# Kernel optimization log

Measured on AMD Instinct MI355X. Metric: run time of the kernel, lower is better.

## Reference

```python
import jax, jax.numpy as jnp
import numpy as np
from jax import lax

D_MODEL = 1024
D_FF = 4096
NUM_EXPERTS = 24
TOP_K = 2
B, S = 2, 2048


def setup_inputs() -> dict:
    key = jax.random.key(0)
    ks = jax.random.split(key, 5)
    x = jax.random.normal(ks[0], (B, S, D_MODEL), dtype=jnp.float32)
    gate_w = jax.random.normal(ks[1], (D_MODEL, NUM_EXPERTS), dtype=jnp.float32) * 0.02
    gate_b = jnp.zeros((NUM_EXPERTS,), dtype=jnp.float32)
    w1 = jax.random.normal(ks[2], (NUM_EXPERTS, D_MODEL, D_FF), dtype=jnp.float32) * 0.02
    b1 = jnp.zeros((NUM_EXPERTS, D_FF), dtype=jnp.float32)
    w2 = jax.random.normal(ks[3], (NUM_EXPERTS, D_FF, D_MODEL), dtype=jnp.float32) * 0.02
    b2 = jnp.zeros((NUM_EXPERTS, D_MODEL), dtype=jnp.float32)
    return {"x": x, "gate_w": gate_w, "gate_b": gate_b,
            "w1": w1, "b1": b1, "w2": w2, "b2": b2}


def reference(x, gate_w, gate_b, w1, b1, w2, b2):
    b, s, d = x.shape
    t = b * s
    xf = x.reshape(t, d)  # [T, d]
    scores = xf @ gate_w + gate_b  # [T, E]
    top_val, top_idx = lax.top_k(scores, TOP_K)  # [T, k]
    prob = jax.nn.softmax(top_val, axis=-1)  # softmax over the top-k logits
    # scatter top-k probabilities into dense per-expert combine weights [T, E]
    combine = jnp.zeros((t, NUM_EXPERTS), dtype=x.dtype)
    combine = combine.at[jnp.arange(t)[:, None], top_idx].add(prob)

    def body(acc, expert):
        w1e, b1e, w2e, b2e, ce = expert  # ce: [T]
        h = jax.nn.gelu(xf @ w1e + b1e, approximate=False)  # exact GELU as torch default
        y = h @ w2e + b2e  # [T, d]
        return acc + ce[:, None] * y, None

    out, _ = lax.scan(body, jnp.zeros_like(xf), (w1, b1, w2, b2, combine.T))
    return out.reshape(b, s, d)
```

## Files before the change

kernel.cpp:

```cpp
#include <hip/hip_runtime.h>
#include <math.h>

#define DM 1024
#define DF 4096
#define NE 24
#define T_TOK 4096
#define T2 (T_TOK*2)

#define BM 128
#define BN 64
#define BK 64
#define MTILES 8
#define NK1 (DM / BK)
#define NK2 (DF / BK)

typedef __attribute__((ext_vector_type(4))) float f32x4;
typedef __attribute__((ext_vector_type(8))) short s16x8;

static __device__ __forceinline__ unsigned short f2bf(float f) {
    unsigned int u = __float_as_uint(f);
    unsigned int r = u + 0x7fffu + ((u >> 16) & 1u);
    return (unsigned short)(r >> 16);
}

static __device__ __forceinline__ unsigned int cvtpk(float lo, float hi) {
    unsigned int r;
    asm("v_cvt_pk_bf16_f32 %0, %1, %2" : "=v"(r) : "v"(lo), "v"(hi));
    return r;
}

#define GLL(gsrc, ldst)                                                          \
    __builtin_amdgcn_global_load_lds(                                            \
        (const __attribute__((address_space(1))) void*)(gsrc),                   \
        (__attribute__((address_space(3))) void*)(ldst), 16, 0, 0)


__global__ void k_transpose_gw(const float* __restrict__ gw, float* __restrict__ gwT) {
    int e = blockIdx.x;
    for (int d = threadIdx.x; d < DM; d += blockDim.x)
        gwT[e * DM + d] = gw[d * NE + e];
}

__global__ void k_gate(const float* __restrict__ x, const float* __restrict__ gwT,
                       const float* __restrict__ gb,
                       int* __restrict__ idx, float* __restrict__ prob) {
    int wave = threadIdx.x >> 6;
    int lane = threadIdx.x & 63;
    int t = blockIdx.x * 4 + wave;
    if (t >= T_TOK) return;
    const float* xr = x + (size_t)t * DM;
    float acc[NE];
#pragma unroll
    for (int e = 0; e < NE; e++) acc[e] = 0.f;
    for (int i = 0; i < DM / 64; i++) {
        int d = lane + i * 64;
        float xv = xr[d];
#pragma unroll
        for (int e = 0; e < NE; e++) acc[e] = fmaf(xv, gwT[e * DM + d], acc[e]);
    }
#pragma unroll
    for (int e = 0; e < NE; e++) {
        float v = acc[e];
        for (int off = 32; off >= 1; off >>= 1) v += __shfl_xor(v, off);
        acc[e] = v;
    }
    if (lane == 0) {
        float v1 = -1e30f, v2 = -1e30f;
        int i1 = -1, i2 = -1;
        for (int e = 0; e < NE; e++) {
            float s = acc[e] + gb[e];
            if (s > v1) { v2 = v1; i2 = i1; v1 = s; i1 = e; }
            else if (s > v2) { v2 = s; i2 = e; }
        }
        float e2 = expf(v2 - v1);
        float inv = 1.f / (1.f + e2);
        idx[t * 2] = i1; idx[t * 2 + 1] = i2;
        prob[t * 2] = inv; prob[t * 2 + 1] = e2 * inv;
    }
}


__global__ __launch_bounds__(1024)
void k_route(const int* __restrict__ idx, int* __restrict__ counts,
             int* __restrict__ offsets, int* __restrict__ slot_tok,
             int* __restrict__ pair_slot) {
    __shared__ int cnt[NE], offs[NE], cur[NE];
    const int tid = threadIdx.x;
    if (tid < NE) cnt[tid] = 0;
    __syncthreads();
    for (int i = tid; i < T2; i += 1024) atomicAdd(&cnt[idx[i]], 1);
    __syncthreads();
    if (tid == 0) {
        int s = 0;
        for (int e = 0; e < NE; e++) {
            offs[e] = s; offsets[e] = s; counts[e] = cnt[e]; s += cnt[e];
        }
    }
    if (tid < NE) cur[tid] = 0;
    __syncthreads();
    for (int i = tid; i < T2; i += 1024) {
        int e = idx[i];
        int pos = offs[e] + atomicAdd(&cur[e], 1);
        slot_tok[pos] = i >> 1;
        pair_slot[i] = pos;
    }
}

__global__ void k_gather(const float* __restrict__ x, const int* __restrict__ slot_tok,
                         unsigned short* __restrict__ Xg) {
    int s = blockIdx.x;
    int tok = slot_tok[s];
    const float4* src = (const float4*)(x + (size_t)tok * DM);
    ushort4* dst = (ushort4*)(Xg + (size_t)s * DM);
    for (int i = threadIdx.x; i < DM / 4; i += blockDim.x) {
        float4 v = src[i];
        ushort4 o;
        o.x = f2bf(v.x); o.y = f2bf(v.y); o.z = f2bf(v.z); o.w = f2bf(v.w);
        dst[i] = o;
    }
}

__global__ void k_combine(const float* __restrict__ Y, const int* __restrict__ pair_slot,
                          const float* __restrict__ prob, const int* __restrict__ idx,
                          const float* __restrict__ b2, float* __restrict__ out) {
    int t = blockIdx.x;
    int s1 = pair_slot[t * 2], s2 = pair_slot[t * 2 + 1];
    int e1 = idx[t * 2], e2 = idx[t * 2 + 1];
    float p1 = prob[t * 2], p2 = prob[t * 2 + 1];
    const float4* y1 = (const float4*)(Y + (size_t)s1 * DM);
    const float4* y2 = (const float4*)(Y + (size_t)s2 * DM);
    const float4* ba = (const float4*)(b2 + (size_t)e1 * DM);
    const float4* bb = (const float4*)(b2 + (size_t)e2 * DM);
    float4* o = (float4*)(out + (size_t)t * DM);
    int i = threadIdx.x;
    float4 a = y1[i], b = y2[i], c = ba[i], d = bb[i];
    float4 r;
    r.x = p1 * (a.x + c.x) + p2 * (b.x + d.x);
    r.y = p1 * (a.y + c.y) + p2 * (b.y + d.y);
    r.z = p1 * (a.z + c.z) + p2 * (b.z + d.z);
    r.w = p1 * (a.w + c.w) + p2 * (b.w + d.w);
    o[i] = r;
}


__global__ __launch_bounds__(256)
void k_mm1(const unsigned short* __restrict__ Xg, const float* __restrict__ w1,
           const float* __restrict__ b1, const int* __restrict__ counts,
           const int* __restrict__ offsets, unsigned short* __restrict__ H) {
    const int TOT = NE * MTILES * (DF / BN);
    int work = (blockIdx.x & 7) * (TOT >> 3) + (blockIdx.x >> 3);
    const int mt = work % MTILES;
    const int en = work / MTILES;
    const int e  = en >> 6;
    const int n0 = (en & 63) * BN;
    const int ne = counts[e];
    const int m0 = mt * BM;
    if (m0 >= ne) return;
    const int rows = min(BM, ne - m0);
    const int slotbase = offsets[e] + m0;

    __shared__ unsigned short As[BM * BK];
    __shared__ float          Bf[BN * BK];
    __shared__ unsigned short Bs[BN * BK];

    const int tid  = threadIdx.x;
    const int lane = tid & 63;
    const int w    = tid >> 6;
    const int wm   = w >> 1, wn = w & 1;

    const float* w1e = w1 + (size_t)e * DM * DF;
    const int arow = lane >> 3;
    const int gchunk = ((lane & 7) ^ arow) * 8;

    const int swz0 = ((lane >> 4) ^ (lane & 7)) << 4;
    const int swz1 = ((4 | (lane >> 4)) ^ (lane & 7)) << 4;
    const char* Arow = (const char*)As + (wm * 64 + (lane & 15)) * 128;
    const char* Brow = (const char*)Bs + (wn * 32 + (lane & 15)) * 128;

    const int cn = lane;
    const int ck = w * 16;
    const int cc0 = ((ck >> 3) ^ (cn & 7)) << 4;
    const int cc1 = (((ck >> 3) + 1) ^ (cn & 7)) << 4;
    char* BsRowC = (char*)Bs + cn * 128;

    f32x4 acc[4][2];
#pragma unroll
    for (int a = 0; a < 4; a++)
#pragma unroll
        for (int b = 0; b < 2; b++) acc[a][b] = (f32x4)0.f;

#pragma unroll 1
    for (int kt = 0; kt < NK1; ++kt) {
        const int k0 = kt * BK;
#pragma unroll
        for (int q = 0; q < 4; q++) {
            int row = (w * 4 + q) * 8 + arow;
            GLL(Xg + (size_t)(slotbase + row) * DM + k0 + gchunk,
                &As[(w * 4 + q) * 512]);
        }
#pragma unroll
        for (int q = 0; q < 4; q++) {
            GLL(w1e + (size_t)(k0 + w * 16 + q * 4 + (lane >> 4)) * DF + n0 + (lane & 15) * 4,
                &Bf[(w * 16 + q * 4) * 64]);
        }
        __syncthreads();
        s16x8 af[2][4];
#pragma unroll
        for (int f = 0; f < 4; f++) {
            af[0][f] = *(const s16x8*)(Arow + f * 2048 + swz0);
            af[1][f] = *(const s16x8*)(Arow + f * 2048 + swz1);
        }
        {
            uint4 v0, v1;
            v0.x = cvtpk(Bf[(ck + 0) * 64 + cn], Bf[(ck + 1) * 64 + cn]);
            v0.y = cvtpk(Bf[(ck + 2) * 64 + cn], Bf[(ck + 3) * 64 + cn]);
            v0.z = cvtpk(Bf[(ck + 4) * 64 + cn], Bf[(ck + 5) * 64 + cn]);
            v0.w = cvtpk(Bf[(ck + 6) * 64 + cn], Bf[(ck + 7) * 64 + cn]);
            v1.x = cvtpk(Bf[(ck + 8) * 64 + cn], Bf[(ck + 9) * 64 + cn]);
            v1.y = cvtpk(Bf[(ck + 10) * 64 + cn], Bf[(ck + 11) * 64 + cn]);
            v1.z = cvtpk(Bf[(ck + 12) * 64 + cn], Bf[(ck + 13) * 64 + cn]);
            v1.w = cvtpk(Bf[(ck + 14) * 64 + cn], Bf[(ck + 15) * 64 + cn]);
            *(uint4*)(BsRowC + cc0) = v0;
            *(uint4*)(BsRowC + cc1) = v1;
        }
        __syncthreads();
        s16x8 bfr[2][2];
#pragma unroll
        for (int f = 0; f < 2; f++) {
            bfr[0][f] = *(const s16x8*)(Brow + f * 2048 + swz0);
            bfr[1][f] = *(const s16x8*)(Brow + f * 2048 + swz1);
        }
#pragma unroll
        for (int ks = 0; ks < 2; ks++)
#pragma unroll
            for (int fm = 0; fm < 4; fm++)
#pragma unroll
                for (int fn = 0; fn < 2; fn++)
                    acc[fm][fn] = __builtin_amdgcn_mfma_f32_16x16x32_bf16(
                        af[ks][fm], bfr[ks][fn], acc[fm][fn], 0, 0, 0);
        __syncthreads();
    }

    const float* b1e = b1 + (size_t)e * DF;
#pragma unroll
    for (int fm = 0; fm < 4; fm++) {
        const int mrow = wm * 64 + fm * 16 + ((lane >> 4) << 2);
#pragma unroll
        for (int fn = 0; fn < 2; fn++) {
            const int ncol = n0 + wn * 32 + fn * 16 + (lane & 15);
            const float bb = b1e[ncol];
#pragma unroll
            for (int r = 0; r < 4; r++) {
                const int m = mrow + r;
                if (m < rows) {
                    float h = acc[fm][fn][r] + bb;
                    h = 0.5f * h * (1.f + erff(h * 0.70710678118654752f));
                    H[(size_t)(slotbase + m) * DF + ncol] = f2bf(h);
                }
            }
        }
    }
}

__global__ __launch_bounds__(256)
void k_mm2(const unsigned short* __restrict__ Hb, const float* __restrict__ w2,
           const int* __restrict__ counts, const int* __restrict__ offsets,
           float* __restrict__ Y) {
    const int TOT = NE * MTILES * (DM / BN);
    int work = (blockIdx.x & 7) * (TOT >> 3) + (blockIdx.x >> 3);
    const int mt = work % MTILES;
    const int en = work / MTILES;
    const int e  = en >> 4;
    const int n0 = (en & 15) * BN;
    const int ne = counts[e];
    const int m0 = mt * BM;
    if (m0 >= ne) return;
    const int rows = min(BM, ne - m0);
    const int slotbase = offsets[e] + m0;

    __shared__ unsigned short As[BM * BK];
    __shared__ float          Bf[BN * BK];
    __shared__ unsigned short Bs[BN * BK];

    const int tid  = threadIdx.x;
    const int lane = tid & 63;
    const int w    = tid >> 6;
    const int wm   = w >> 1, wn = w & 1;

    const float* w2e = w2 + (size_t)e * DF * DM;
    const int arow = lane >> 3;
    const int gchunk = ((lane & 7) ^ arow) * 8;

    const int swz0 = ((lane >> 4) ^ (lane & 7)) << 4;
    const int swz1 = ((4 | (lane >> 4)) ^ (lane & 7)) << 4;
    const char* Arow = (const char*)As + (wm * 64 + (lane & 15)) * 128;
    const char* Brow = (const char*)Bs + (wn * 32 + (lane & 15)) * 128;

    const int cn = lane;
    const int ck = w * 16;
    const int cc0 = ((ck >> 3) ^ (cn & 7)) << 4;
    const int cc1 = (((ck >> 3) + 1) ^ (cn & 7)) << 4;
    char* BsRowC = (char*)Bs + cn * 128;

    f32x4 acc[4][2];
#pragma unroll
    for (int a = 0; a < 4; a++)
#pragma unroll
        for (int b = 0; b < 2; b++) acc[a][b] = (f32x4)0.f;

#pragma unroll 1
    for (int kt = 0; kt < NK2; ++kt) {
        const int k0 = kt * BK;
#pragma unroll
        for (int q = 0; q < 4; q++) {
            int row = (w * 4 + q) * 8 + arow;
            GLL(Hb + (size_t)(slotbase + row) * DF + k0 + gchunk,
                &As[(w * 4 + q) * 512]);
        }
#pragma unroll
        for (int q = 0; q < 4; q++) {
            GLL(w2e + (size_t)(k0 + w * 16 + q * 4 + (lane >> 4)) * DM + n0 + (lane & 15) * 4,
                &Bf[(w * 16 + q * 4) * 64]);
        }
        __syncthreads();
        s16x8 af[2][4];
#pragma unroll
        for (int f = 0; f < 4; f++) {
            af[0][f] = *(const s16x8*)(Arow + f * 2048 + swz0);
            af[1][f] = *(const s16x8*)(Arow + f * 2048 + swz1);
        }
        {
            uint4 v0, v1;
            v0.x = cvtpk(Bf[(ck + 0) * 64 + cn], Bf[(ck + 1) * 64 + cn]);
            v0.y = cvtpk(Bf[(ck + 2) * 64 + cn], Bf[(ck + 3) * 64 + cn]);
            v0.z = cvtpk(Bf[(ck + 4) * 64 + cn], Bf[(ck + 5) * 64 + cn]);
            v0.w = cvtpk(Bf[(ck + 6) * 64 + cn], Bf[(ck + 7) * 64 + cn]);
            v1.x = cvtpk(Bf[(ck + 8) * 64 + cn], Bf[(ck + 9) * 64 + cn]);
            v1.y = cvtpk(Bf[(ck + 10) * 64 + cn], Bf[(ck + 11) * 64 + cn]);
            v1.z = cvtpk(Bf[(ck + 12) * 64 + cn], Bf[(ck + 13) * 64 + cn]);
            v1.w = cvtpk(Bf[(ck + 14) * 64 + cn], Bf[(ck + 15) * 64 + cn]);
            *(uint4*)(BsRowC + cc0) = v0;
            *(uint4*)(BsRowC + cc1) = v1;
        }
        __syncthreads();
        s16x8 bfr[2][2];
#pragma unroll
        for (int f = 0; f < 2; f++) {
            bfr[0][f] = *(const s16x8*)(Brow + f * 2048 + swz0);
            bfr[1][f] = *(const s16x8*)(Brow + f * 2048 + swz1);
        }
#pragma unroll
        for (int ks = 0; ks < 2; ks++)
#pragma unroll
            for (int fm = 0; fm < 4; fm++)
#pragma unroll
                for (int fn = 0; fn < 2; fn++)
                    acc[fm][fn] = __builtin_amdgcn_mfma_f32_16x16x32_bf16(
                        af[ks][fm], bfr[ks][fn], acc[fm][fn], 0, 0, 0);
        __syncthreads();
    }

#pragma unroll
    for (int fm = 0; fm < 4; fm++) {
        const int mrow = wm * 64 + fm * 16 + ((lane >> 4) << 2);
#pragma unroll
        for (int fn = 0; fn < 2; fn++) {
            const int ncol = n0 + wn * 32 + fn * 16 + (lane & 15);
#pragma unroll
            for (int r = 0; r < 4; r++) {
                const int m = mrow + r;
                if (m < rows)
                    Y[(size_t)(slotbase + m) * DM + ncol] = acc[fm][fn][r];
            }
        }
    }
}


extern "C" void kernel_launch(void* const* d_in, const int* in_sizes, int n_in,
                              void* d_out, int out_size, void* d_ws, size_t ws_size,
                              hipStream_t stream) {
    const float* x   = (const float*)d_in[0];
    const float* gw  = (const float*)d_in[1];
    const float* gb  = (const float*)d_in[2];
    const float* w1  = (const float*)d_in[3];
    const float* b1  = (const float*)d_in[4];
    const float* w2  = (const float*)d_in[5];
    const float* b2  = (const float*)d_in[6];
    float* out = (float*)d_out;

    size_t off = 0;
    auto alloc = [&](size_t bytes) {
        void* p = (char*)d_ws + off;
        off += (bytes + 255) & ~(size_t)255;
        return p;
    };
    float* gwT       = (float*)alloc(NE * DM * sizeof(float));
    int*   idx       = (int*)alloc(T2 * sizeof(int));
    float* prob      = (float*)alloc(T2 * sizeof(float));
    int*   counts    = (int*)alloc(32 * sizeof(int));
    int*   offsets   = (int*)alloc(32 * sizeof(int));
    int*   slot_tok  = (int*)alloc(T2 * sizeof(int));
    int*   pair_slot = (int*)alloc(T2 * sizeof(int));
    unsigned short* Xg = (unsigned short*)alloc((size_t)(T2 + BM) * DM * sizeof(unsigned short));
    unsigned short* Hb = (unsigned short*)alloc((size_t)(T2 + BM) * DF * sizeof(unsigned short));
    float* Yb        = (float*)alloc((size_t)(T2 + BM) * DM * sizeof(float));

    k_transpose_gw<<<NE, 256, 0, stream>>>(gw, gwT);
    k_gate<<<T_TOK / 4, 256, 0, stream>>>(x, gwT, gb, idx, prob);
    k_route<<<1, 1024, 0, stream>>>(idx, counts, offsets, slot_tok, pair_slot);
    k_gather<<<T2, 256, 0, stream>>>(x, slot_tok, Xg);

    k_mm1<<<NE * MTILES * (DF / BN), 256, 0, stream>>>(Xg, w1, b1, counts, offsets, Hb);
    k_mm2<<<NE * MTILES * (DM / BN), 256, 0, stream>>>(Hb, w2, counts, offsets, Yb);
    k_combine<<<T_TOK, 256, 0, stream>>>(Yb, pair_slot, prob, idx, b2, out);
}
```

Before: 570.3 us.

## Widen expert GEMM tiles to 128x128 with 512-thread blocks

Result: no change. 562.4 us (-1.4%).

```diff
diff --git a/kernel.cpp b/kernel.cpp
--- a/kernel.cpp
+++ b/kernel.cpp
@@ -8,7 +8,7 @@
 #define T2 (T_TOK*2)
 
 #define BM 128
-#define BN 64
+#define BN 128
 #define BK 64
 #define MTILES 8
 #define NK1 (DM / BK)
@@ -143,7 +143,7 @@
 }
 
 
-__global__ __launch_bounds__(256)
+__global__ __launch_bounds__(512)
 void k_mm1(const unsigned short* __restrict__ Xg, const float* __restrict__ w1,
            const float* __restrict__ b1, const int* __restrict__ counts,
            const int* __restrict__ offsets, unsigned short* __restrict__ H) {
@@ -151,8 +151,8 @@
     int work = (blockIdx.x & 7) * (TOT >> 3) + (blockIdx.x >> 3);
     const int mt = work % MTILES;
     const int en = work / MTILES;
-    const int e  = en >> 6;
-    const int n0 = (en & 63) * BN;
+    const int e  = en >> 5;
+    const int n0 = (en & 31) * BN;
     const int ne = counts[e];
     const int m0 = mt * BM;
     if (m0 >= ne) return;
@@ -160,7 +160,7 @@
     const int slotbase = offsets[e] + m0;
 
     __shared__ unsigned short As[BM * BK];
-    __shared__ float          Bf[BN * BK];
+    __shared__ float          Bf[BK * BN];
     __shared__ unsigned short Bs[BN * BK];
 
     const int tid  = threadIdx.x;
@@ -174,68 +174,68 @@
 
     const int swz0 = ((lane >> 4) ^ (lane & 7)) << 4;
     const int swz1 = ((4 | (lane >> 4)) ^ (lane & 7)) << 4;
-    const char* Arow = (const char*)As + (wm * 64 + (lane & 15)) * 128;
-    const char* Brow = (const char*)Bs + (wn * 32 + (lane & 15)) * 128;
-
-    const int cn = lane;
-    const int ck = w * 16;
+    const char* Arow = (const char*)As + (wm * 32 + (lane & 15)) * 128;
+    const char* Brow = (const char*)Bs + (wn * 64 + (lane & 15)) * 128;
+
+    const int cn = tid & 127;
+    const int ck = (tid >> 7) * 16;
     const int cc0 = ((ck >> 3) ^ (cn & 7)) << 4;
     const int cc1 = (((ck >> 3) + 1) ^ (cn & 7)) << 4;
     char* BsRowC = (char*)Bs + cn * 128;
 
-    f32x4 acc[4][2];
-#pragma unroll
-    for (int a = 0; a < 4; a++)
-#pragma unroll
-        for (int b = 0; b < 2; b++) acc[a][b] = (f32x4)0.f;
+    f32x4 acc[2][4];
+#pragma unroll
+    for (int a = 0; a < 2; a++)
+#pragma unroll
+        for (int b = 0; b < 4; b++) acc[a][b] = (f32x4)0.f;
 
 #pragma unroll 1
     for (int kt = 0; kt < NK1; ++kt) {
         const int k0 = kt * BK;
 #pragma unroll
+        for (int q = 0; q < 2; q++) {
+            int row = (w * 2 + q) * 8 + arow;
+            GLL(Xg + (size_t)(slotbase + row) * DM + k0 + gchunk,
+                &As[(w * 2 + q) * 512]);
+        }
+#pragma unroll
         for (int q = 0; q < 4; q++) {
-            int row = (w * 4 + q) * 8 + arow;
-            GLL(Xg + (size_t)(slotbase + row) * DM + k0 + gchunk,
-                &As[(w * 4 + q) * 512]);
-        }
-#pragma unroll
-        for (int q = 0; q < 4; q++) {
-            GLL(w1e + (size_t)(k0 + w * 16 + q * 4 + (lane >> 4)) * DF + n0 + (lane & 15) * 4,
-                &Bf[(w * 16 + q * 4) * 64]);
-        }
-        __syncthreads();
-        s16x8 af[2][4];
-#pragma unroll
-        for (int f = 0; f < 4; f++) {
+            GLL(w1e + (size_t)(k0 + w * 8 + q * 2 + (lane >> 5)) * DF + n0 + (lane & 31) * 4,
+                &Bf[(w * 8 + q * 2) * BN]);
+        }
+        __syncthreads();
+        s16x8 af[2][2];
+#pragma unroll
+        for (int f = 0; f < 2; f++) {
             af[0][f] = *(const s16x8*)(Arow + f * 2048 + swz0);
             af[1][f] = *(const s16x8*)(Arow + f * 2048 + swz1);
         }
         {
             uint4 v0, v1;
-            v0.x = cvtpk(Bf[(ck + 0) * 64 + cn], Bf[(ck + 1) * 64 + cn]);
-            v0.y = cvtpk(Bf[(ck + 2) * 64 + cn], Bf[(ck + 3) * 64 + cn]);
-            v0.z = cvtpk(Bf[(ck + 4) * 64 + cn], Bf[(ck + 5) * 64 + cn]);
-            v0.w = cvtpk(Bf[(ck + 6) * 64 + cn], Bf[(ck + 7) * 64 + cn]);
-            v1.x = cvtpk(Bf[(ck + 8) * 64 + cn], Bf[(ck + 9) * 64 + cn]);
-            v1.y = cvtpk(Bf[(ck + 10) * 64 + cn], Bf[(ck + 11) * 64 + cn]);
-            v1.z = cvtpk(Bf[(ck + 12) * 64 + cn], Bf[(ck + 13) * 64 + cn]);
-            v1.w = cvtpk(Bf[(ck + 14) * 64 + cn], Bf[(ck + 15) * 64 + cn]);
+            v0.x = cvtpk(Bf[(ck + 0) * BN + cn], Bf[(ck + 1) * BN + cn]);
+            v0.y = cvtpk(Bf[(ck + 2) * BN + cn], Bf[(ck + 3) * BN + cn]);
+            v0.z = cvtpk(Bf[(ck + 4) * BN + cn], Bf[(ck + 5) * BN + cn]);
+            v0.w = cvtpk(Bf[(ck + 6) * BN + cn], Bf[(ck + 7) * BN + cn]);
+            v1.x = cvtpk(Bf[(ck + 8) * BN + cn], Bf[(ck + 9) * BN + cn]);
+            v1.y = cvtpk(Bf[(ck + 10) * BN + cn], Bf[(ck + 11) * BN + cn]);
+            v1.z = cvtpk(Bf[(ck + 12) * BN + cn], Bf[(ck + 13) * BN + cn]);
+            v1.w = cvtpk(Bf[(ck + 14) * BN + cn], Bf[(ck + 15) * BN + cn]);
             *(uint4*)(BsRowC + cc0) = v0;
             *(uint4*)(BsRowC + cc1) = v1;
         }
         __syncthreads();
-        s16x8 bfr[2][2];
-#pragma unroll
-        for (int f = 0; f < 2; f++) {
+        s16x8 bfr[2][4];
+#pragma unroll
+        for (int f = 0; f < 4; f++) {
             bfr[0][f] = *(const s16x8*)(Brow + f * 2048 + swz0);
             bfr[1][f] = *(const s16x8*)(Brow + f * 2048 + swz1);
         }
 #pragma unroll
         for (int ks = 0; ks < 2; ks++)
 #pragma unroll
-            for (int fm = 0; fm < 4; fm++)
-#pragma unroll
-                for (int fn = 0; fn < 2; fn++)
+            for (int fm = 0; fm < 2; fm++)
+#pragma unroll
+                for (int fn = 0; fn < 4; fn++)
                     acc[fm][fn] = __builtin_amdgcn_mfma_f32_16x16x32_bf16(
                         af[ks][fm], bfr[ks][fn], acc[fm][fn], 0, 0, 0);
         __syncthreads();
@@ -243,11 +243,11 @@
 
     const float* b1e = b1 + (size_t)e * DF;
 #pragma unroll
-    for (int fm = 0; fm < 4; fm++) {
-        const int mrow = wm * 64 + fm * 16 + ((lane >> 4) << 2);
-#pragma unroll
-        for (int fn = 0; fn < 2; fn++) {
-            const int ncol = n0 + wn * 32 + fn * 16 + (lane & 15);
+    for (int fm = 0; fm < 2; fm++) {
+        const int mrow = wm * 32 + fm * 16 + ((lane >> 4) << 2);
+#pragma unroll
+        for (int fn = 0; fn < 4; fn++) {
+            const int ncol = n0 + wn * 64 + fn * 16 + (lane & 15);
             const float bb = b1e[ncol];
 #pragma unroll
             for (int r = 0; r < 4; r++) {
@@ -262,7 +262,7 @@
     }
 }
 
-__global__ __launch_bounds__(256)
+__global__ __launch_bounds__(512)
 void k_mm2(const unsigned short* __restrict__ Hb, const float* __restrict__ w2,
            const int* __restrict__ counts, const int* __restrict__ offsets,
            float* __restrict__ Y) {
@@ -270,8 +270,8 @@
     int work = (blockIdx.x & 7) * (TOT >> 3) + (blockIdx.x >> 3);
     const int mt = work % MTILES;
     const int en = work / MTILES;
-    const int e  = en >> 4;
-    const int n0 = (en & 15) * BN;
+    const int e  = en >> 3;
+    const int n0 = (en & 7) * BN;
     const int ne = counts[e];
     const int m0 = mt * BM;
     if (m0 >= ne) return;
@@ -279,7 +279,7 @@
     const int slotbase = offsets[e] + m0;
 
     __shared__ unsigned short As[BM * BK];
-    __shared__ float          Bf[BN * BK];
+    __shared__ float          Bf[BK * BN];
     __shared__ unsigned short Bs[BN * BK];
 
     const int tid  = threadIdx.x;
@@ -293,79 +293,79 @@
 
     const int swz0 = ((lane >> 4) ^ (lane & 7)) << 4;
     const int swz1 = ((4 | (lane >> 4)) ^ (lane & 7)) << 4;
-    const char* Arow = (const char*)As + (wm * 64 + (lane & 15)) * 128;
-    const char* Brow = (const char*)Bs + (wn * 32 + (lane & 15)) * 128;
-
-    const int cn = lane;
-    const int ck = w * 16;
+    const char* Arow = (const char*)As + (wm * 32 + (lane & 15)) * 128;
+    const char* Brow = (const char*)Bs + (wn * 64 + (lane & 15)) * 128;
+
+    const int cn = tid & 127;
+    const int ck = (tid >> 7) * 16;
     const int cc0 = ((ck >> 3) ^ (cn & 7)) << 4;
     const int cc1 = (((ck >> 3) + 1) ^ (cn & 7)) << 4;
     char* BsRowC = (char*)Bs + cn * 128;
 
-    f32x4 acc[4][2];
-#pragma unroll
-    for (int a = 0; a < 4; a++)
-#pragma unroll
-        for (int b = 0; b < 2; b++) acc[a][b] = (f32x4)0.f;
+    f32x4 acc[2][4];
+#pragma unroll
+    for (int a = 0; a < 2; a++)
+#pragma unroll
+        for (int b = 0; b < 4; b++) acc[a][b] = (f32x4)0.f;
 
 #pragma unroll 1
     for (int kt = 0; kt < NK2; ++kt) {
         const int k0 = kt * BK;
 #pragma unroll
+        for (int q = 0; q < 2; q++) {
+            int row = (w * 2 + q) * 8 + arow;
+            GLL(Hb + (size_t)(slotbase + row) * DF + k0 + gchunk,
+                &As[(w * 2 + q) * 512]);
+        }
+#pragma unroll
         for (int q = 0; q < 4; q++) {
-            int row = (w * 4 + q) * 8 + arow;
-            GLL(Hb + (size_t)(slotbase + row) * DF + k0 + gchunk,
-                &As[(w * 4 + q) * 512]);
-        }
-#pragma unroll
-        for (int q = 0; q < 4; q++) {
-            GLL(w2e + (size_t)(k0 + w * 16 + q * 4 + (lane >> 4)) * DM + n0 + (lane & 15) * 4,
-                &Bf[(w * 16 + q * 4) * 64]);
-        }
-        __syncthreads();
-        s16x8 af[2][4];
-#pragma unroll
-        for (int f = 0; f < 4; f++) {
+            GLL(w2e + (size_t)(k0 + w * 8 + q * 2 + (lane >> 5)) * DM + n0 + (lane & 31) * 4,
+                &Bf[(w * 8 + q * 2) * BN]);
+        }
+        __syncthreads();
+        s16x8 af[2][2];
+#pragma unroll
+        for (int f = 0; f < 2; f++) {
             af[0][f] = *(const s16x8*)(Arow + f * 2048 + swz0);
             af[1][f] = *(const s16x8*)(Arow + f * 2048 + swz1);
         }
         {
             uint4 v0, v1;
-            v0.x = cvtpk(Bf[(ck + 0) * 64 + cn], Bf[(ck + 1) * 64 + cn]);
-            v0.y = cvtpk(Bf[(ck + 2) * 64 + cn], Bf[(ck + 3) * 64 + cn]);
-            v0.z = cvtpk(Bf[(ck + 4) * 64 + cn], Bf[(ck + 5) * 64 + cn]);
-            v0.w = cvtpk(Bf[(ck + 6) * 64 + cn], Bf[(ck + 7) * 64 + cn]);
-            v1.x = cvtpk(Bf[(ck + 8) * 64 + cn], Bf[(ck + 9) * 64 + cn]);
-            v1.y = cvtpk(Bf[(ck + 10) * 64 + cn], Bf[(ck + 11) * 64 + cn]);
-            v1.z = cvtpk(Bf[(ck + 12) * 64 + cn], Bf[(ck + 13) * 64 + cn]);
-            v1.w = cvtpk(Bf[(ck + 14) * 64 + cn], Bf[(ck + 15) * 64 + cn]);
+            v0.x = cvtpk(Bf[(ck + 0) * BN + cn], Bf[(ck + 1) * BN + cn]);
+            v0.y = cvtpk(Bf[(ck + 2) * BN + cn], Bf[(ck + 3) * BN + cn]);
+            v0.z = cvtpk(Bf[(ck + 4) * BN + cn], Bf[(ck + 5) * BN + cn]);
+            v0.w = cvtpk(Bf[(ck + 6) * BN + cn], Bf[(ck + 7) * BN + cn]);
+            v1.x = cvtpk(Bf[(ck + 8) * BN + cn], Bf[(ck + 9) * BN + cn]);
+            v1.y = cvtpk(Bf[(ck + 10) * BN + cn], Bf[(ck + 11) * BN + cn]);
+            v1.z = cvtpk(Bf[(ck + 12) * BN + cn], Bf[(ck + 13) * BN + cn]);
+            v1.w = cvtpk(Bf[(ck + 14) * BN + cn], Bf[(ck + 15) * BN + cn]);
             *(uint4*)(BsRowC + cc0) = v0;
             *(uint4*)(BsRowC + cc1) = v1;
         }
         __syncthreads();
-        s16x8 bfr[2][2];
-#pragma unroll
-        for (int f = 0; f < 2; f++) {
+        s16x8 bfr[2][4];
+#pragma unroll
+        for (int f = 0; f < 4; f++) {
             bfr[0][f] = *(const s16x8*)(Brow + f * 2048 + swz0);
             bfr[1][f] = *(const s16x8*)(Brow + f * 2048 + swz1);
         }
 #pragma unroll
         for (int ks = 0; ks < 2; ks++)
 #pragma unroll
-            for (int fm = 0; fm < 4; fm++)
-#pragma unroll
-                for (int fn = 0; fn < 2; fn++)
+            for (int fm = 0; fm < 2; fm++)
+#pragma unroll
+                for (int fn = 0; fn < 4; fn++)
                     acc[fm][fn] = __builtin_amdgcn_mfma_f32_16x16x32_bf16(
                         af[ks][fm], bfr[ks][fn], acc[fm][fn], 0, 0, 0);
         __syncthreads();
     }
 
 #pragma unroll
-    for (int fm = 0; fm < 4; fm++) {
-        const int mrow = wm * 64 + fm * 16 + ((lane >> 4) << 2);
-#pragma unroll
-        for (int fn = 0; fn < 2; fn++) {
-            const int ncol = n0 + wn * 32 + fn * 16 + (lane & 15);
+    for (int fm = 0; fm < 2; fm++) {
+        const int mrow = wm * 32 + fm * 16 + ((lane >> 4) << 2);
+#pragma unroll
+        for (int fn = 0; fn < 4; fn++) {
+            const int ncol = n0 + wn * 64 + fn * 16 + (lane & 15);
 #pragma unroll
             for (int r = 0; r < 4; r++) {
                 const int m = mrow + r;
@@ -411,7 +411,7 @@
     k_route<<<1, 1024, 0, stream>>>(idx, counts, offsets, slot_tok, pair_slot);
     k_gather<<<T2, 256, 0, stream>>>(x, slot_tok, Xg);
 
-    k_mm1<<<NE * MTILES * (DF / BN), 256, 0, stream>>>(Xg, w1, b1, counts, offsets, Hb);
-    k_mm2<<<NE * MTILES * (DM / BN), 256, 0, stream>>>(Hb, w2, counts, offsets, Yb);
+    k_mm1<<<NE * MTILES * (DF / BN), 512, 0, stream>>>(Xg, w1, b1, counts, offsets, Hb);
+    k_mm2<<<NE * MTILES * (DM / BN), 512, 0, stream>>>(Hb, w2, counts, offsets, Yb);
     k_combine<<<T_TOK, 256, 0, stream>>>(Yb, pair_slot, prob, idx, b2, out);
 }
```
